# Kernel optimization log

Measured on AMD Instinct MI355X. Metric: run time of the kernel, lower is better.

## Reference

```python
import jax, jax.numpy as jnp
import numpy as np

N_NODES = 50000
N_EDGES = 800000
N_GRAPHS = 512
IN_CH, HID_CH, OUT_CH, N_CLASSES = 128, 64, 64, 10


def gcn_conv(x, src, dst, ew, W, b, n_nodes):
    """PyG GCNConv: add self-loops (weight 1), symmetric normalization, x @ W, scatter-add at dst, + bias."""
    xw = x @ W  # [N, out]
    loop = jnp.arange(n_nodes, dtype=src.dtype)
    src_f = jnp.concatenate([src, loop])
    dst_f = jnp.concatenate([dst, loop])
    ew_f = jnp.concatenate([ew, jnp.ones((n_nodes,), dtype=ew.dtype)])
    deg = jax.ops.segment_sum(ew_f, dst_f, num_segments=n_nodes)  # [N]
    dinv = jnp.where(deg > 0, jax.lax.rsqrt(deg), 0.0)
    norm = dinv[src_f] * ew_f * dinv[dst_f]  # [E+N]
    msg = norm[:, None] * xw[src_f]  # gather + scale
    out = jax.ops.segment_sum(msg, dst_f, num_segments=n_nodes)  # scatter-add
    return out + b


def setup_inputs() -> dict:
    key = jax.random.key(0)
    ks = jax.random.split(key, 12)
    x = jax.random.normal(ks[0], (N_NODES, IN_CH), dtype=jnp.float32)
    edge_index = jax.random.randint(ks[1], (2, N_EDGES), 0, N_NODES, dtype=jnp.int64)
    edge_attr = jax.random.uniform(ks[2], (N_EDGES,), dtype=jnp.float32)
    batch = jnp.sort(jax.random.randint(ks[3], (N_NODES,), 0, N_GRAPHS, dtype=jnp.int64))
    def glorot(k, shape):
        lim = np.sqrt(6.0 / (shape[0] + shape[1]))
        return jax.random.uniform(k, shape, jnp.float32, -lim, lim)
    W1 = glorot(ks[4], (IN_CH, HID_CH))
    b1 = jnp.zeros((HID_CH,), jnp.float32)
    W2 = glorot(ks[5], (HID_CH, OUT_CH))
    b2 = jnp.zeros((OUT_CH,), jnp.float32)
    LW1 = glorot(ks[6], (OUT_CH, 32))
    Lb1 = jnp.zeros((32,), jnp.float32)
    LW2 = glorot(ks[7], (32, N_CLASSES))
    Lb2 = jnp.zeros((N_CLASSES,), jnp.float32)
    return {"x": x, "edge_index": edge_index, "edge_attr": edge_attr, "batch": batch,
            "W1": W1, "b1": b1, "W2": W2, "b2": b2,
            "LW1": LW1, "Lb1": Lb1, "LW2": LW2, "Lb2": Lb2}


def reference(x, edge_index, edge_attr, batch, W1, b1, W2, b2, LW1, Lb1, LW2, Lb2):
    src, dst = edge_index[0], edge_index[1]
    h = gcn_conv(x, src, dst, edge_attr, W1, b1, N_NODES)
    h = jax.nn.relu(h)
    h = gcn_conv(h, src, dst, edge_attr, W2, b2, N_NODES)
    # global mean pool over graphs
    sums = jax.ops.segment_sum(h, batch, num_segments=N_GRAPHS)  # [G, OUT]
    cnt = jax.ops.segment_sum(jnp.ones((N_NODES,), h.dtype), batch, num_segments=N_GRAPHS)
    pooled = sums / jnp.maximum(cnt, 1.0)[:, None]
    # head (dropout treated as identity for deterministic reference)
    h1 = pooled @ LW1 + Lb1
    return h1 @ LW2 + Lb2
```

## Files before the change

kernel.cpp:

```cpp
#include <hip/hip_runtime.h>
#include <hip/hip_bf16.h>

static constexpr int NN = 50000;
static constexpr int NE = 800000;
static constexpr int NG = 512;
static constexpr int NB = 196;
static constexpr int GEMM_BLOCKS = (NN + 63) / 64;
static constexpr int HB = 128;
static_assert(NN % 16 == 0, "agg_gemm assumes exact 16-node blocks");
static_assert(NN % 4 == 0, "agg kernels assume exact 4-node blocks");

__device__ __forceinline__ float bfu(ushort u) {
    return __uint_as_float((unsigned)u << 16);
}
__device__ __forceinline__ ushort fbf(float f) {
    return __hip_bfloat16_raw(__float2bfloat16(f)).x;
}


__global__ void zero_kernel(float* __restrict__ p, int n) {
    int i = blockIdx.x * blockDim.x + threadIdx.x;
    if (i < n) p[i] = 0.f;
}

template <int K>
__device__ __forceinline__ void gemm_body(const float* __restrict__ X,
                                          const float* __restrict__ W,
                                          ushort* __restrict__ out,
                                          int row0, float Xs[][68], float Ws[][64]) {
    int tx = threadIdx.x & 15, ty = threadIdx.x >> 4;
    float acc[4][4] = {};
    for (int kb = 0; kb < K; kb += 64) {
        __syncthreads();
        for (int i = threadIdx.x; i < 1024; i += 256) {
            int kk = i >> 4, c4 = i & 15;
            *(float4*)&Ws[kk][c4 * 4] = *(const float4*)&W[(kb + kk) * 64 + c4 * 4];
        }
        for (int i = threadIdx.x; i < 1024; i += 256) {
            int r = i >> 4, k4 = i & 15;
            int gr = row0 + r; if (gr >= NN) gr = NN - 1;
            float4 v = *(const float4*)(X + (long long)gr * K + kb + k4 * 4);
            *(float4*)&Xs[r][k4 * 4] = v;
        }
        __syncthreads();
#pragma unroll
        for (int k4 = 0; k4 < 16; ++k4) {
            float4 w0 = *(const float4*)&Ws[k4 * 4 + 0][tx * 4];
            float4 w1 = *(const float4*)&Ws[k4 * 4 + 1][tx * 4];
            float4 w2 = *(const float4*)&Ws[k4 * 4 + 2][tx * 4];
            float4 w3 = *(const float4*)&Ws[k4 * 4 + 3][tx * 4];
            float4 x0 = *(const float4*)&Xs[ty * 4 + 0][k4 * 4];
            float4 x1 = *(const float4*)&Xs[ty * 4 + 1][k4 * 4];
            float4 x2 = *(const float4*)&Xs[ty * 4 + 2][k4 * 4];
            float4 x3 = *(const float4*)&Xs[ty * 4 + 3][k4 * 4];
#define GCN_ROW(j, xv) \
            acc[j][0]=fmaf(xv.x,w0.x,acc[j][0]); acc[j][1]=fmaf(xv.x,w0.y,acc[j][1]); \
            acc[j][2]=fmaf(xv.x,w0.z,acc[j][2]); acc[j][3]=fmaf(xv.x,w0.w,acc[j][3]); \
            acc[j][0]=fmaf(xv.y,w1.x,acc[j][0]); acc[j][1]=fmaf(xv.y,w1.y,acc[j][1]); \
            acc[j][2]=fmaf(xv.y,w1.z,acc[j][2]); acc[j][3]=fmaf(xv.y,w1.w,acc[j][3]); \
            acc[j][0]=fmaf(xv.z,w2.x,acc[j][0]); acc[j][1]=fmaf(xv.z,w2.y,acc[j][1]); \
            acc[j][2]=fmaf(xv.z,w2.z,acc[j][2]); acc[j][3]=fmaf(xv.z,w2.w,acc[j][3]); \
            acc[j][0]=fmaf(xv.w,w3.x,acc[j][0]); acc[j][1]=fmaf(xv.w,w3.y,acc[j][1]); \
            acc[j][2]=fmaf(xv.w,w3.z,acc[j][2]); acc[j][3]=fmaf(xv.w,w3.w,acc[j][3]);
            GCN_ROW(0, x0)
            GCN_ROW(1, x1)
            GCN_ROW(2, x2)
            GCN_ROW(3, x3)
#undef GCN_ROW
        }
    }
#pragma unroll
    for (int j = 0; j < 4; ++j) {
        int r = row0 + ty * 4 + j;
        if (r < NN) {
            ushort4 sv;
            sv.x = fbf(acc[j][0]); sv.y = fbf(acc[j][1]);
            sv.z = fbf(acc[j][2]); sv.w = fbf(acc[j][3]);
            *(ushort4*)(out + (long long)r * 64 + tx * 4) = sv;
        }
    }
}

__global__ __launch_bounds__(256) void hist_gemm_kernel(const int* __restrict__ dst,
                                                        const float* __restrict__ ew,
                                                        unsigned long long* __restrict__ h,
                                                        int* __restrict__ rank,
                                                        const float* __restrict__ X,
                                                        const float* __restrict__ W,
                                                        ushort* __restrict__ out) {
    __shared__ float Xs[64][68];
    __shared__ float Ws[64][64];
    if (blockIdx.x < HB) {
        for (int e = blockIdx.x * 256 + threadIdx.x; e < NE; e += HB * 256) {
            int d = dst[e];
            unsigned int fx = __float2uint_rn(ew[e] * 1048576.0f);
            unsigned long long pack = (1ULL << 40) | (unsigned long long)fx;
            unsigned long long old = atomicAdd(&h[d], pack);
            rank[e] = (int)(old >> 40);
        }
        return;
    }
    gemm_body<128>(X, W, out, (blockIdx.x - HB) * 64, Xs, Ws);
}

__global__ __launch_bounds__(256) void dinv_scanA_kernel(const unsigned long long* __restrict__ h,
                                                         float* __restrict__ dinv,
                                                         int* __restrict__ partial) {
    int i = blockIdx.x * 256 + threadIdx.x;
    int cnt = 0;
    if (i < NN) {
        unsigned long long v = h[i];
        cnt = (int)(v >> 40);
        float deg = (float)(v & ((1ULL << 40) - 1)) * (1.0f / 1048576.0f) + 1.0f;
        dinv[i] = 1.0f / sqrtf(deg);
    }
    __shared__ int wsum[4];
    int lane = threadIdx.x & 63, wid = threadIdx.x >> 6;
    int v = cnt;
#pragma unroll
    for (int off = 32; off > 0; off >>= 1) v += __shfl_down(v, (unsigned)off, 64);
    if (lane == 0) wsum[wid] = v;
    __syncthreads();
    if (threadIdx.x == 0) partial[blockIdx.x] = wsum[0] + wsum[1] + wsum[2] + wsum[3];
}

__device__ __forceinline__ int block_scan_inclusive(int v, int* wtot) {
    int lane = threadIdx.x & 63, wid = threadIdx.x >> 6;
    int inc = v;
#pragma unroll
    for (int off = 1; off < 64; off <<= 1) {
        int n = __shfl_up(inc, (unsigned)off, 64);
        if (lane >= off) inc += n;
    }
    if (lane == 63) wtot[wid] = inc;
    __syncthreads();
    int add = 0;
    for (int w = 0; w < wid; ++w) add += wtot[w];
    return inc + add;
}

__global__ __launch_bounds__(256) void scanC_bounds_kernel(const unsigned long long* __restrict__ h,
                                                           const int* __restrict__ partial,
                                                           int* __restrict__ rowptr,
                                                           const int* __restrict__ batch,
                                                           int* __restrict__ gbeg,
                                                           int* __restrict__ gend) {
    __shared__ int wtot[4];
    __shared__ int poff_s;
    int t = threadIdx.x;
    if (t < 64) {
        int s = 0;
        for (int i = t; i < (int)blockIdx.x; i += 64) s += partial[i];
#pragma unroll
        for (int off = 32; off > 0; off >>= 1) s += __shfl_down(s, (unsigned)off, 64);
        if (t == 0) poff_s = s;
    }
    int i = blockIdx.x * 256 + t;
    int v = (i < NN) ? (int)(h[i] >> 40) : 0;
    int incl = block_scan_inclusive(v, wtot);
    if (i < NN) {
        rowptr[i + 1] = poff_s + incl;
        int g = batch[i];
        if (i == 0 || batch[i - 1] != g) gbeg[g] = i;
        if (i == NN - 1 || batch[i + 1] != g) gend[g] = i + 1;
    }
    if (i == 0) rowptr[0] = 0;
}

__global__ __launch_bounds__(256) void scatter_kernel(const int* __restrict__ src,
                                                      const int* __restrict__ dst,
                                                      const float* __restrict__ ew,
                                                      const float* __restrict__ dinv,
                                                      const int* __restrict__ rowptr,
                                                      const int* __restrict__ rank,
                                                      int2* __restrict__ epack) {
    int e = blockIdx.x * blockDim.x + threadIdx.x;
    if (e >= NE) return;
    int s = src[e], d = dst[e];
    int pos = rowptr[d] + rank[e];
    float coef = dinv[s] * ew[e];
    epack[pos] = make_int2(s, __float_as_int(coef));
}

__global__ __launch_bounds__(256) void agg_gemm_kernel(const ushort* __restrict__ xw,
                                                       const int* __restrict__ rowptr,
                                                       const int2* __restrict__ epack,
                                                       const float* __restrict__ dinv,
                                                       const float* __restrict__ bias,
                                                       const float* __restrict__ W2,
                                                       ushort* __restrict__ xw2) {
    __shared__ float h1s[4][4][64];
    int w = threadIdx.x >> 6;
    int lane = threadIdx.x & 63;
    int e8 = lane >> 3;
    int l8 = lane & 7;
    int base = blockIdx.x * 16 + w * 4;
    for (int t = 0; t < 4; ++t) {
        int node = base + t;
        int beg = rowptr[node], end = rowptr[node + 1];
        float a0 = 0.f, a1 = 0.f, a2 = 0.f, a3 = 0.f;
        float a4 = 0.f, a5 = 0.f, a6 = 0.f, a7 = 0.f;
        for (int j = beg + e8; j < end; j += 8) {
            int2 p = epack[j];
            uint4 v = *(const uint4*)(xw + p.x * 64 + l8 * 8);
            float wt = __int_as_float(p.y);
            a0 = fmaf(wt, __uint_as_float(v.x << 16), a0);
            a1 = fmaf(wt, __uint_as_float(v.x & 0xffff0000u), a1);
            a2 = fmaf(wt, __uint_as_float(v.y << 16), a2);
            a3 = fmaf(wt, __uint_as_float(v.y & 0xffff0000u), a3);
            a4 = fmaf(wt, __uint_as_float(v.z << 16), a4);
            a5 = fmaf(wt, __uint_as_float(v.z & 0xffff0000u), a5);
            a6 = fmaf(wt, __uint_as_float(v.w << 16), a6);
            a7 = fmaf(wt, __uint_as_float(v.w & 0xffff0000u), a7);
        }
#define RED(x) x += __shfl_xor(x, 8); x += __shfl_xor(x, 16); x += __shfl_xor(x, 32);
        RED(a0) RED(a1) RED(a2) RED(a3) RED(a4) RED(a5) RED(a6) RED(a7)
#undef RED
        if (e8 == 0) {
            float di = dinv[node];
            float d2 = di * di;
            uint4 us = *(const uint4*)(xw + node * 64 + l8 * 8);
            float4 bv0 = *(const float4*)(bias + l8 * 8);
            float4 bv1 = *(const float4*)(bias + l8 * 8 + 4);
            float o0 = fmaf(di, a0, fmaf(d2, __uint_as_float(us.x << 16), bv0.x));
            float o1 = fmaf(di, a1, fmaf(d2, __uint_as_float(us.x & 0xffff0000u), bv0.y));
            float o2 = fmaf(di, a2, fmaf(d2, __uint_as_float(us.y << 16), bv0.z));
            float o3 = fmaf(di, a3, fmaf(d2, __uint_as_float(us.y & 0xffff0000u), bv0.w));
            float o4 = fmaf(di, a4, fmaf(d2, __uint_as_float(us.z << 16), bv1.x));
            float o5 = fmaf(di, a5, fmaf(d2, __uint_as_float(us.z & 0xffff0000u), bv1.y));
            float o6 = fmaf(di, a6, fmaf(d2, __uint_as_float(us.w << 16), bv1.z));
            float o7 = fmaf(di, a7, fmaf(d2, __uint_as_float(us.w & 0xffff0000u), bv1.w));
            *(float4*)&h1s[w][t][l8 * 8]     = make_float4(fmaxf(o0, 0.f), fmaxf(o1, 0.f),
                                                           fmaxf(o2, 0.f), fmaxf(o3, 0.f));
            *(float4*)&h1s[w][t][l8 * 8 + 4] = make_float4(fmaxf(o4, 0.f), fmaxf(o5, 0.f),
                                                           fmaxf(o6, 0.f), fmaxf(o7, 0.f));
        }
    }
    __syncthreads();
    float w2c[64];
#pragma unroll
    for (int k = 0; k < 64; ++k) w2c[k] = W2[k * 64 + lane];
#pragma unroll
    for (int t = 0; t < 4; ++t) {
        float acc = 0.f;
#pragma unroll
        for (int k4 = 0; k4 < 16; ++k4) {
            float4 hv = *(const float4*)&h1s[w][t][k4 * 4];
            acc = fmaf(hv.x, w2c[k4 * 4 + 0], acc);
            acc = fmaf(hv.y, w2c[k4 * 4 + 1], acc);
            acc = fmaf(hv.z, w2c[k4 * 4 + 2], acc);
            acc = fmaf(hv.w, w2c[k4 * 4 + 3], acc);
        }
        xw2[(base + t) * 64 + lane] = fbf(acc);
    }
}

template <bool RELU>
__global__ __launch_bounds__(256) void agg_kernel(const ushort* __restrict__ xw,
                                                  const int* __restrict__ rowptr,
                                                  const int2* __restrict__ epack,
                                                  const float* __restrict__ dinv,
                                                  const float* __restrict__ bias,
                                                  ushort* __restrict__ out) {
    int node = blockIdx.x * 4 + (threadIdx.x >> 6);
    int lane = threadIdx.x & 63;
    int e8 = lane >> 3;
    int l8 = lane & 7;
    int beg = rowptr[node], end = rowptr[node + 1];
    float a0 = 0.f, a1 = 0.f, a2 = 0.f, a3 = 0.f;
    float a4 = 0.f, a5 = 0.f, a6 = 0.f, a7 = 0.f;
    for (int j = beg + e8; j < end; j += 8) {
        int2 p = epack[j];
        uint4 v = *(const uint4*)(xw + p.x * 64 + l8 * 8);
        float w = __int_as_float(p.y);
        a0 = fmaf(w, __uint_as_float(v.x << 16), a0);
        a1 = fmaf(w, __uint_as_float(v.x & 0xffff0000u), a1);
        a2 = fmaf(w, __uint_as_float(v.y << 16), a2);
        a3 = fmaf(w, __uint_as_float(v.y & 0xffff0000u), a3);
        a4 = fmaf(w, __uint_as_float(v.z << 16), a4);
        a5 = fmaf(w, __uint_as_float(v.z & 0xffff0000u), a5);
        a6 = fmaf(w, __uint_as_float(v.w << 16), a6);
        a7 = fmaf(w, __uint_as_float(v.w & 0xffff0000u), a7);
    }
#define RED(x) x += __shfl_xor(x, 8); x += __shfl_xor(x, 16); x += __shfl_xor(x, 32);
    RED(a0) RED(a1) RED(a2) RED(a3) RED(a4) RED(a5) RED(a6) RED(a7)
#undef RED
    if (e8 == 0) {
        float di = dinv[node];
        float d2 = di * di;
        uint4 us = *(const uint4*)(xw + node * 64 + l8 * 8);
        float4 bv0 = *(const float4*)(bias + l8 * 8);
        float4 bv1 = *(const float4*)(bias + l8 * 8 + 4);
        float o0 = fmaf(di, a0, fmaf(d2, __uint_as_float(us.x << 16), bv0.x));
        float o1 = fmaf(di, a1, fmaf(d2, __uint_as_float(us.x & 0xffff0000u), bv0.y));
        float o2 = fmaf(di, a2, fmaf(d2, __uint_as_float(us.y << 16), bv0.z));
        float o3 = fmaf(di, a3, fmaf(d2, __uint_as_float(us.y & 0xffff0000u), bv0.w));
        float o4 = fmaf(di, a4, fmaf(d2, __uint_as_float(us.z << 16), bv1.x));
        float o5 = fmaf(di, a5, fmaf(d2, __uint_as_float(us.z & 0xffff0000u), bv1.y));
        float o6 = fmaf(di, a6, fmaf(d2, __uint_as_float(us.w << 16), bv1.z));
        float o7 = fmaf(di, a7, fmaf(d2, __uint_as_float(us.w & 0xffff0000u), bv1.w));
        if (RELU) {
            o0 = fmaxf(o0, 0.f); o1 = fmaxf(o1, 0.f); o2 = fmaxf(o2, 0.f); o3 = fmaxf(o3, 0.f);
            o4 = fmaxf(o4, 0.f); o5 = fmaxf(o5, 0.f); o6 = fmaxf(o6, 0.f); o7 = fmaxf(o7, 0.f);
        }
        uint4 sv;
        sv.x = (unsigned)fbf(o0) | ((unsigned)fbf(o1) << 16);
        sv.y = (unsigned)fbf(o2) | ((unsigned)fbf(o3) << 16);
        sv.z = (unsigned)fbf(o4) | ((unsigned)fbf(o5) << 16);
        sv.w = (unsigned)fbf(o6) | ((unsigned)fbf(o7) << 16);
        *(uint4*)(out + node * 64 + l8 * 8) = sv;
    }
}

__global__ __launch_bounds__(256) void poolhead_kernel(const ushort* __restrict__ h,
                                                       const int* __restrict__ gbeg,
                                                       const int* __restrict__ gend,
                                                       const float* __restrict__ LW1,
                                                       const float* __restrict__ Lb1,
                                                       const float* __restrict__ LW2,
                                                       const float* __restrict__ Lb2,
                                                       float* __restrict__ out) {
    __shared__ float pp[4][64];
    __shared__ float p[64];
    __shared__ float t1[32];
    int g = blockIdx.x, t = threadIdx.x;
    int lane = t & 63, wid = t >> 6;
    int b = gbeg[g], e = gend[g];
    float acc = 0.f;
    for (int i = b + wid; i < e; i += 4) acc += bfu(h[i * 64 + lane]);
    pp[wid][lane] = acc;
    __syncthreads();
    if (t < 64) {
        float s = pp[0][t] + pp[1][t] + pp[2][t] + pp[3][t];
        p[t] = s / fmaxf((float)(e - b), 1.0f);
    }
    __syncthreads();
    if (t < 32) {
        float a = Lb1[t];
#pragma unroll
        for (int k = 0; k < 64; ++k) a = fmaf(p[k], LW1[k * 32 + t], a);
        t1[t] = a;
    }
    __syncthreads();
    if (t < 10) {
        float a = Lb2[t];
#pragma unroll
        for (int j = 0; j < 32; ++j) a = fmaf(t1[j], LW2[j * 10 + t], a);
        out[g * 10 + t] = a;
    }
}


extern "C" void kernel_launch(void* const* d_in, const int* in_sizes, int n_in,
                              void* d_out, int out_size, void* d_ws, size_t ws_size,
                              hipStream_t stream) {
    const float* x     = (const float*)d_in[0];
    const int*   ei    = (const int*)d_in[1];
    const float* ew    = (const float*)d_in[2];
    const int*   batch = (const int*)d_in[3];
    const float* W1    = (const float*)d_in[4];
    const float* b1    = (const float*)d_in[5];
    const float* W2    = (const float*)d_in[6];
    const float* b2    = (const float*)d_in[7];
    const float* LW1   = (const float*)d_in[8];
    const float* Lb1   = (const float*)d_in[9];
    const float* LW2   = (const float*)d_in[10];
    const float* Lb2   = (const float*)d_in[11];

    const int* src = ei;
    const int* dst = ei + NE;

    float* ws = (float*)d_ws;
    unsigned long long* h64 = (unsigned long long*)ws;
    int*   gbeg   = (int*)(ws + 100096);
    int*   gend   = (int*)(ws + 100608);
    float* dinv   = ws + 101120;
    int*   rowptr = (int*)(ws + 151168);
    int*   partial= (int*)(ws + 201248);
    int2*  epack  = (int2*)(ws + 201504);
    ushort* xwA   = (ushort*)(ws + 1801504);
    ushort* xwB   = (ushort*)(ws + 3401504);
    int*   rank   = (int*)(ws + 5001504);
    ushort* h2    = xwA;

    zero_kernel<<<(101120 + 255) / 256, 256, 0, stream>>>(ws, 101120);

    hist_gemm_kernel<<<HB + GEMM_BLOCKS, 256, 0, stream>>>(dst, ew, h64, rank, x, W1, xwA);
    dinv_scanA_kernel<<<NB, 256, 0, stream>>>(h64, dinv, partial);
    scanC_bounds_kernel<<<NB, 256, 0, stream>>>(h64, partial, rowptr, batch, gbeg, gend);
    scatter_kernel<<<(NE + 255) / 256, 256, 0, stream>>>(src, dst, ew, dinv, rowptr,
                                                         rank, epack);

    agg_gemm_kernel<<<NN / 16, 256, 0, stream>>>(xwA, rowptr, epack, dinv, b1, W2, xwB);

    agg_kernel<false><<<NN / 4, 256, 0, stream>>>(xwB, rowptr, epack, dinv, b2, h2);

    poolhead_kernel<<<NG, 256, 0, stream>>>(h2, gbeg, gend, LW1, Lb1, LW2, Lb2, (float*)d_out);
}
```

Before: 230.8 us.

## Fuse scan and scatter stages with grid barriers; dynamic histogram work distribution

Merges the dinv/partial-sum, prefix-scan/bounds and edge-scatter kernels into one persistent kernel of NB blocks that uses software grid barriers built on atomic counters, removing two kernel launches and their gaps. The histogram phase now hands out edge chunks through an atomic cursor, and GEMM blocks join in once their tile is done, which balances load between histogram and GEMM work. The grid barrier assumes all 196 blocks are co-resident, which holds on this GPU but is not guaranteed in general. The scatter phase now runs on only 196 blocks with a grid-stride loop instead of a full-width launch.

New measurement: 281.4 us. +21.9%, slower.

```diff
diff --git a/kernel.cpp b/kernel.cpp
--- a/kernel.cpp
+++ b/kernel.cpp
@@ -21,6 +21,17 @@
 __global__ void zero_kernel(float* __restrict__ p, int n) {
     int i = blockIdx.x * blockDim.x + threadIdx.x;
     if (i < n) p[i] = 0.f;
+}
+
+__device__ __forceinline__ void grid_barrier(int* bar, int nblocks) {
+    __syncthreads();
+    if (threadIdx.x == 0) {
+        __threadfence();
+        atomicAdd(bar, 1);
+        while (atomicAdd(bar, 0) < nblocks) __builtin_amdgcn_s_sleep(8);
+        __threadfence();
+    }
+    __syncthreads();
 }
 
 template <int K>
@@ -85,28 +96,61 @@
                                                         const float* __restrict__ ew,
                                                         unsigned long long* __restrict__ h,
                                                         int* __restrict__ rank,
+                                                        int* __restrict__ cursor,
                                                         const float* __restrict__ X,
                                                         const float* __restrict__ W,
                                                         ushort* __restrict__ out) {
     __shared__ float Xs[64][68];
     __shared__ float Ws[64][64];
-    if (blockIdx.x < HB) {
-        for (int e = blockIdx.x * 256 + threadIdx.x; e < NE; e += HB * 256) {
+    __shared__ int s_e0;
+    if (blockIdx.x >= HB)
+        gemm_body<128>(X, W, out, (blockIdx.x - HB) * 64, Xs, Ws);
+    for (;;) {
+        if (threadIdx.x == 0) s_e0 = atomicAdd(cursor, 256);
+        __syncthreads();
+        int e0 = s_e0;
+        __syncthreads();
+        if (e0 >= NE) break;
+        int e = e0 + threadIdx.x;
+        if (e < NE) {
             int d = dst[e];
             unsigned int fx = __float2uint_rn(ew[e] * 1048576.0f);
             unsigned long long pack = (1ULL << 40) | (unsigned long long)fx;
             unsigned long long old = atomicAdd(&h[d], pack);
             rank[e] = (int)(old >> 40);
         }
-        return;
-    }
-    gemm_body<128>(X, W, out, (blockIdx.x - HB) * 64, Xs, Ws);
-}
-
-__global__ __launch_bounds__(256) void dinv_scanA_kernel(const unsigned long long* __restrict__ h,
-                                                         float* __restrict__ dinv,
-                                                         int* __restrict__ partial) {
-    int i = blockIdx.x * 256 + threadIdx.x;
+    }
+}
+
+__device__ __forceinline__ int block_scan_inclusive(int v, int* wtot) {
+    int lane = threadIdx.x & 63, wid = threadIdx.x >> 6;
+    int inc = v;
+#pragma unroll
+    for (int off = 1; off < 64; off <<= 1) {
+        int n = __shfl_up(inc, (unsigned)off, 64);
+        if (lane >= off) inc += n;
+    }
+    if (lane == 63) wtot[wid] = inc;
+    __syncthreads();
+    int add = 0;
+    for (int w = 0; w < wid; ++w) add += wtot[w];
+    return inc + add;
+}
+
+__global__ __launch_bounds__(256) void scan_scatter_kernel(
+        const unsigned long long* __restrict__ h,
+        float* __restrict__ dinv, int* __restrict__ partial,
+        int* __restrict__ rowptr, const int* __restrict__ batch,
+        int* __restrict__ gbeg, int* __restrict__ gend,
+        const int* __restrict__ src, const int* __restrict__ dst,
+        const float* __restrict__ ew, const int* __restrict__ rank,
+        int2* __restrict__ epack, int* __restrict__ bar) {
+    __shared__ int wsum[4];
+    __shared__ int wtot[4];
+    __shared__ int poff_s;
+    int t = threadIdx.x;
+    int i = blockIdx.x * 256 + t;
+    int lane = t & 63, wid = t >> 6;
     int cnt = 0;
     if (i < NN) {
         unsigned long long v = h[i];
@@ -114,50 +158,21 @@
         float deg = (float)(v & ((1ULL << 40) - 1)) * (1.0f / 1048576.0f) + 1.0f;
         dinv[i] = 1.0f / sqrtf(deg);
     }
-    __shared__ int wsum[4];
-    int lane = threadIdx.x & 63, wid = threadIdx.x >> 6;
     int v = cnt;
 #pragma unroll
     for (int off = 32; off > 0; off >>= 1) v += __shfl_down(v, (unsigned)off, 64);
     if (lane == 0) wsum[wid] = v;
     __syncthreads();
-    if (threadIdx.x == 0) partial[blockIdx.x] = wsum[0] + wsum[1] + wsum[2] + wsum[3];
-}
-
-__device__ __forceinline__ int block_scan_inclusive(int v, int* wtot) {
-    int lane = threadIdx.x & 63, wid = threadIdx.x >> 6;
-    int inc = v;
-#pragma unroll
-    for (int off = 1; off < 64; off <<= 1) {
-        int n = __shfl_up(inc, (unsigned)off, 64);
-        if (lane >= off) inc += n;
-    }
-    if (lane == 63) wtot[wid] = inc;
-    __syncthreads();
-    int add = 0;
-    for (int w = 0; w < wid; ++w) add += wtot[w];
-    return inc + add;
-}
-
-__global__ __launch_bounds__(256) void scanC_bounds_kernel(const unsigned long long* __restrict__ h,
-                                                           const int* __restrict__ partial,
-                                                           int* __restrict__ rowptr,
-                                                           const int* __restrict__ batch,
-                                                           int* __restrict__ gbeg,
-                                                           int* __restrict__ gend) {
-    __shared__ int wtot[4];
-    __shared__ int poff_s;
-    int t = threadIdx.x;
+    if (t == 0) partial[blockIdx.x] = wsum[0] + wsum[1] + wsum[2] + wsum[3];
+    grid_barrier(&bar[0], NB);
     if (t < 64) {
         int s = 0;
-        for (int i = t; i < (int)blockIdx.x; i += 64) s += partial[i];
+        for (int j = t; j < (int)blockIdx.x; j += 64) s += partial[j];
 #pragma unroll
         for (int off = 32; off > 0; off >>= 1) s += __shfl_down(s, (unsigned)off, 64);
         if (t == 0) poff_s = s;
     }
-    int i = blockIdx.x * 256 + t;
-    int v = (i < NN) ? (int)(h[i] >> 40) : 0;
-    int incl = block_scan_inclusive(v, wtot);
+    int incl = block_scan_inclusive(cnt, wtot);
     if (i < NN) {
         rowptr[i + 1] = poff_s + incl;
         int g = batch[i];
@@ -165,21 +180,13 @@
         if (i == NN - 1 || batch[i + 1] != g) gend[g] = i + 1;
     }
     if (i == 0) rowptr[0] = 0;
-}
-
-__global__ __launch_bounds__(256) void scatter_kernel(const int* __restrict__ src,
-                                                      const int* __restrict__ dst,
-                                                      const float* __restrict__ ew,
-                                                      const float* __restrict__ dinv,
-                                                      const int* __restrict__ rowptr,
-                                                      const int* __restrict__ rank,
-                                                      int2* __restrict__ epack) {
-    int e = blockIdx.x * blockDim.x + threadIdx.x;
-    if (e >= NE) return;
-    int s = src[e], d = dst[e];
-    int pos = rowptr[d] + rank[e];
-    float coef = dinv[s] * ew[e];
-    epack[pos] = make_int2(s, __float_as_int(coef));
+    grid_barrier(&bar[1], NB);
+    for (int e = blockIdx.x * 256 + t; e < NE; e += NB * 256) {
+        int s = src[e], d = dst[e];
+        int pos = rowptr[d] + rank[e];
+        float coef = dinv[s] * ew[e];
+        epack[pos] = make_int2(s, __float_as_int(coef));
+    }
 }
 
 __global__ __launch_bounds__(256) void agg_gemm_kernel(const ushort* __restrict__ xw,
@@ -374,22 +381,23 @@
     unsigned long long* h64 = (unsigned long long*)ws;
     int*   gbeg   = (int*)(ws + 100096);
     int*   gend   = (int*)(ws + 100608);
-    float* dinv   = ws + 101120;
-    int*   rowptr = (int*)(ws + 151168);
-    int*   partial= (int*)(ws + 201248);
-    int2*  epack  = (int2*)(ws + 201504);
-    ushort* xwA   = (ushort*)(ws + 1801504);
-    ushort* xwB   = (ushort*)(ws + 3401504);
-    int*   rank   = (int*)(ws + 5001504);
+    int*   ctl    = (int*)(ws + 101120);
+    float* dinv   = ws + 101128;
+    int*   rowptr = (int*)(ws + 151128);
+    int*   partial= (int*)(ws + 201132);
+    int2*  epack  = (int2*)(ws + 201328);
+    ushort* xwA   = (ushort*)(ws + 1801328);
+    ushort* xwB   = (ushort*)(ws + 3401328);
+    int*   rank   = (int*)(ws + 5001328);
     ushort* h2    = xwA;
 
-    zero_kernel<<<(101120 + 255) / 256, 256, 0, stream>>>(ws, 101120);
-
-    hist_gemm_kernel<<<HB + GEMM_BLOCKS, 256, 0, stream>>>(dst, ew, h64, rank, x, W1, xwA);
-    dinv_scanA_kernel<<<NB, 256, 0, stream>>>(h64, dinv, partial);
-    scanC_bounds_kernel<<<NB, 256, 0, stream>>>(h64, partial, rowptr, batch, gbeg, gend);
-    scatter_kernel<<<(NE + 255) / 256, 256, 0, stream>>>(src, dst, ew, dinv, rowptr,
-                                                         rank, epack);
+    zero_kernel<<<(101128 + 255) / 256, 256, 0, stream>>>(ws, 101128);
+
+    hist_gemm_kernel<<<HB + GEMM_BLOCKS, 256, 0, stream>>>(dst, ew, h64, rank, &ctl[0],
+                                                           x, W1, xwA);
+    scan_scatter_kernel<<<NB, 256, 0, stream>>>(h64, dinv, partial, rowptr, batch,
+                                                gbeg, gend, src, dst, ew, rank,
+                                                epack, &ctl[1]);
 
     agg_gemm_kernel<<<NN / 16, 256, 0, stream>>>(xwA, rowptr, epack, dinv, b1, W2, xwB);
 
```
